# Optimization experiments

Measured on AMD Instinct MI355X. Metric: run time of the kernel, lower is better.

## Reference

```python
import jax, jax.numpy as jnp
import numpy as np

B, S, H_IN = 32, 1024, 1024
N_BLK, D_BLK = 64, 16
H_OUT = N_BLK * D_BLK  # 1024


def setup_inputs() -> dict:
    key = jax.random.key(0)
    ks = jax.random.split(key, 10)
    u = lambda k, shape: jax.random.uniform(k, shape, jnp.float32, -0.1, 0.1)
    return {
        "x": jax.random.normal(ks[0], (B, S, H_IN), jnp.float32),
        "h_0": jnp.zeros((B, H_OUT), jnp.float32),
        "c_0": jnp.zeros((B, N_BLK, D_BLK), jnp.float32),
        "Wi": u(ks[1], (N_BLK, H_IN)),
        "bi": jax.random.uniform(ks[2], (N_BLK,), jnp.float32, -1.0, 0.0),
        "Wo": u(ks[3], (N_BLK, H_IN)),
        "bo": jax.random.uniform(ks[4], (N_BLK,), jnp.float32, -1.0, 0.0),
        "Wg": u(ks[5], (H_OUT, H_IN)),
        "bg": u(ks[6], (H_OUT,)),
        "Ui": u(ks[7], (N_BLK, H_OUT)),
        "Uo": u(ks[8], (N_BLK, H_OUT)),
        "Ug": u(ks[9], (H_OUT, H_OUT)),
    }


def _lstm1997(x, h_0, c_0, Wi, bi, Wo, bo, Wg, bg, Ui, Uo, Ug):
    b, s, _ = x.shape
    n_blk, d_blk = c_0.shape[1], c_0.shape[2]
    # Precompute input-to-gate projections for all timesteps (same math, hoisted).
    xi = jnp.einsum("bsi,ni->bsn", x, Wi) + bi          # (B,S,nBlk)
    xo = jnp.einsum("bsi,ni->bsn", x, Wo) + bo          # (B,S,nBlk)
    xg = jnp.einsum("bsi,hi->bsh", x, Wg) + bg          # (B,S,hOut)

    def step(carry, inp):
        h, c = carry                                    # (B,hOut), (B,nBlk,dBlk)
        xi_t, xo_t, xg_t = inp
        i_t = jax.nn.sigmoid(xi_t + h @ Ui.T)           # (B,nBlk)
        o_t = jax.nn.sigmoid(xo_t + h @ Uo.T)           # (B,nBlk)
        g_t = jnp.tanh(xg_t + h @ Ug.T).reshape(b, n_blk, d_blk)
        c_new = c + i_t[:, :, None] * g_t               # (B,nBlk,dBlk)
        h_new = (o_t[:, :, None] * jnp.tanh(c_new)).reshape(b, n_blk * d_blk)
        return (h_new, c_new), (c_new, h_new)

    xs = (jnp.swapaxes(xi, 0, 1), jnp.swapaxes(xo, 0, 1), jnp.swapaxes(xg, 0, 1))
    _, (c_seq, h_seq) = jax.lax.scan(step, (h_0, c_0), xs)
    c = jnp.swapaxes(c_seq, 0, 1)                       # (B,S,nBlk,dBlk)
    h = jnp.swapaxes(h_seq, 0, 1)                       # (B,S,hOut)
    return c, h


def reference(x, h_0, c_0, Wi, bi, Wo, bo, Wg, bg, Ui, Uo, Ug):
    return _lstm1997(x, h_0, c_0, Wi, bi, Wo, bo, Wg, bg, Ui, Uo, Ug)
```

## Files before the change

kernel.cpp:

```cpp
#include <hip/hip_runtime.h>
#include <stdint.h>

#define B_    32
#define S_    1024
#define HIN   1024
#define NBLK  64
#define DBLK  16
#define HOUT  1024
#define NGATE 1152
#define NSLICE 32

typedef __attribute__((ext_vector_type(8))) __bf16 bf16x8;
typedef __attribute__((ext_vector_type(4))) float  f32x4;
typedef __attribute__((ext_vector_type(4))) unsigned int u32x4;

__device__ __forceinline__ unsigned short f2bf(float f) {
    union { float f; unsigned u; } v; v.f = f;
    return (unsigned short)((v.u + 0x7fffu + ((v.u >> 16) & 1u)) >> 16);
}
__device__ __forceinline__ float bf2f(unsigned short h) {
    union { unsigned u; float f; } v; v.u = ((unsigned)h) << 16; return v.f;
}
__device__ __forceinline__ void split1(float f, unsigned short& hi, unsigned short& lo) {
    hi = f2bf(f);
    lo = f2bf(f - bf2f(hi));
}

__device__ __forceinline__ int slice_row(int slice, int r) {
    return (r < 32) ? (128 + slice * 32 + r)
         : (r < 34) ? (slice * 2 + (r - 32))
                    : (64 + slice * 2 + (r - 34));
}


__global__ void k_init(const float* __restrict__ Wi, const float* __restrict__ Wo,
                       const float* __restrict__ Wg,
                       const float* __restrict__ Ui, const float* __restrict__ Uo,
                       const float* __restrict__ Ug, const float* __restrict__ h0,
                       unsigned short* __restrict__ WsH, unsigned short* __restrict__ WsL,
                       unsigned short* __restrict__ UsH, unsigned short* __restrict__ UsL,
                       unsigned short* __restrict__ hbH, unsigned short* __restrict__ hbL)
{
    int idx = blockIdx.x * 256 + threadIdx.x;
    const int nW = NGATE * HOUT / 4;
    float4 v; unsigned short *dH, *dL;
    if (idx < nW) {
        int f = idx * 4; int row = f >> 10, k = f & 1023;
        const float* src = (row < 64)  ? (Wi + (size_t)row * HIN)
                         : (row < 128) ? (Wo + (size_t)(row - 64) * HIN)
                                       : (Wg + (size_t)(row - 128) * HIN);
        v = *(const float4*)(src + k);
        dH = WsH + f; dL = WsL + f;
    } else if (idx < 2 * nW) {
        int f = (idx - nW) * 4; int row = f >> 10, k = f & 1023;
        const float* src = (row < 64)  ? (Ui + (size_t)row * HOUT)
                         : (row < 128) ? (Uo + (size_t)(row - 64) * HOUT)
                                       : (Ug + (size_t)(row - 128) * HOUT);
        v = *(const float4*)(src + k);
        dH = UsH + f; dL = UsL + f;
    } else {
        int f = (idx - 2 * nW) * 4;
        if (f >= B_ * HOUT) return;
        v = *(const float4*)(h0 + f);
        int b = f >> 10, c = f & 1023;
        int g = b >> 4, r = b & 15;
        int off = g * 16384 + (c >> 3) * 128 + r * 8 + (c & 7);
        unsigned short th[4], tl[4];
        split1(v.x, th[0], tl[0]); split1(v.y, th[1], tl[1]);
        split1(v.z, th[2], tl[2]); split1(v.w, th[3], tl[3]);
        __hip_atomic_store((unsigned*)(hbH + off), (unsigned)th[0] | ((unsigned)th[1] << 16),
                           __ATOMIC_RELAXED, __HIP_MEMORY_SCOPE_AGENT);
        __hip_atomic_store((unsigned*)(hbH + off) + 1, (unsigned)th[2] | ((unsigned)th[3] << 16),
                           __ATOMIC_RELAXED, __HIP_MEMORY_SCOPE_AGENT);
        __hip_atomic_store((unsigned*)(hbL + off), (unsigned)tl[0] | ((unsigned)tl[1] << 16),
                           __ATOMIC_RELAXED, __HIP_MEMORY_SCOPE_AGENT);
        __hip_atomic_store((unsigned*)(hbL + off) + 1, (unsigned)tl[2] | ((unsigned)tl[3] << 16),
                           __ATOMIC_RELAXED, __HIP_MEMORY_SCOPE_AGENT);
        return;
    }
    unsigned short th[4], tl[4];
    split1(v.x, th[0], tl[0]); split1(v.y, th[1], tl[1]);
    split1(v.z, th[2], tl[2]); split1(v.w, th[3], tl[3]);
    *(uint2*)dH = *(const uint2*)th;
    *(uint2*)dL = *(const uint2*)tl;
}

#define BM 128
#define BN 128
#define BK 32
#define LDP 56

__global__ __launch_bounds__(256) void k_gates(
    const float* __restrict__ x,
    const unsigned short* __restrict__ WsH, const unsigned short* __restrict__ WsL,
    const float* __restrict__ bi, const float* __restrict__ bo, const float* __restrict__ bg,
    float* __restrict__ c_out, float* __restrict__ h_out)
{
    __shared__ unsigned short AlH[BM][LDP], AlL[BM][LDP];
    __shared__ unsigned short BlH[BN][LDP], BlL[BN][LDP];
    const int tid  = threadIdx.x;
    const int bm   = blockIdx.x, bn = blockIdx.y;
    const int wave = tid >> 6,  lane = tid & 63;
    const int l15  = lane & 15, l4 = lane >> 4;
    const int wm   = wave >> 1, wn = wave & 1;
    const int rbase = tid >> 3;
    const int c4    = (tid & 7) * 4;

    f32x4 acc[4][4] = {};

    for (int kk = 0; kk < HIN; kk += BK) {
        #pragma unroll
        for (int i = 0; i < 4; ++i) {
            int row = rbase + 32 * i;
            float4 v = *(const float4*)(x + (size_t)(bm * BM + row) * HIN + kk + c4);
            unsigned short th[4], tl[4];
            split1(v.x, th[0], tl[0]); split1(v.y, th[1], tl[1]);
            split1(v.z, th[2], tl[2]); split1(v.w, th[3], tl[3]);
            *(uint2*)&AlH[row][c4] = *(const uint2*)th;
            *(uint2*)&AlL[row][c4] = *(const uint2*)tl;
            int n = bn * BN + row;
            *(uint2*)&BlH[row][c4] = *(const uint2*)(WsH + (size_t)n * HIN + kk + c4);
            *(uint2*)&BlL[row][c4] = *(const uint2*)(WsL + (size_t)n * HIN + kk + c4);
        }
        __syncthreads();
        uint4 ah[4], al[4], bh4[4], bl4[4];
        #pragma unroll
        for (int mi = 0; mi < 4; ++mi) {
            ah[mi] = *(const uint4*)&AlH[wm * 64 + mi * 16 + l15][l4 * 8];
            al[mi] = *(const uint4*)&AlL[wm * 64 + mi * 16 + l15][l4 * 8];
        }
        #pragma unroll
        for (int ni = 0; ni < 4; ++ni) {
            bh4[ni] = *(const uint4*)&BlH[wn * 64 + ni * 16 + l15][l4 * 8];
            bl4[ni] = *(const uint4*)&BlL[wn * 64 + ni * 16 + l15][l4 * 8];
        }
        #pragma unroll
        for (int mi = 0; mi < 4; ++mi) {
            #pragma unroll
            for (int ni = 0; ni < 4; ++ni) {
                acc[mi][ni] = __builtin_amdgcn_mfma_f32_16x16x32_bf16(
                    __builtin_bit_cast(bf16x8, ah[mi]), __builtin_bit_cast(bf16x8, bh4[ni]),
                    acc[mi][ni], 0, 0, 0);
                acc[mi][ni] = __builtin_amdgcn_mfma_f32_16x16x32_bf16(
                    __builtin_bit_cast(bf16x8, ah[mi]), __builtin_bit_cast(bf16x8, bl4[ni]),
                    acc[mi][ni], 0, 0, 0);
                acc[mi][ni] = __builtin_amdgcn_mfma_f32_16x16x32_bf16(
                    __builtin_bit_cast(bf16x8, al[mi]), __builtin_bit_cast(bf16x8, bh4[ni]),
                    acc[mi][ni], 0, 0, 0);
            }
        }
        __syncthreads();
    }

    #pragma unroll
    for (int ni = 0; ni < 4; ++ni) {
        int n = bn * BN + wn * 64 + ni * 16 + l15;
        float bv = (n < 64) ? bi[n] : (n < 128) ? bo[n - 64] : bg[n - 128];
        #pragma unroll
        for (int mi = 0; mi < 4; ++mi) {
            #pragma unroll
            for (int r = 0; r < 4; ++r) {
                int m = bm * BM + wm * 64 + mi * 16 + l4 * 4 + r;
                float val = acc[mi][ni][r] + bv;
                if (n >= 128) {
                    h_out[(size_t)m * HOUT + (n - 128)] = val;
                } else if (n < 64) {
                    c_out[((size_t)m * NBLK + n) * DBLK + 0] = val;
                } else {
                    c_out[((size_t)m * NBLK + (n - 64)) * DBLK + 1] = val;
                }
            }
        }
    }
}

__global__ __launch_bounds__(256, 1) void k_rec(
    const float* __restrict__ c0,
    float* __restrict__ c_out, float* __restrict__ h_out,
    const unsigned short* __restrict__ UsH, const unsigned short* __restrict__ UsL,
    unsigned short* __restrict__ hbH, unsigned short* __restrict__ hbL,
    unsigned int* __restrict__ flags)
{
    __shared__ unsigned short Wlo[37][1032];
    __shared__ float preW[4][16][53];

    const int tid   = threadIdx.x;
    const int slice = blockIdx.x & 31;
    const int group = blockIdx.x >> 5;
    const int wave  = tid >> 6, lane = tid & 63;
    const int l15   = lane & 15, l4 = lane >> 4;

    for (int idx = tid; idx < 37 * 128; idx += 256) {
        int row = idx >> 7, c8 = idx & 127;
        uint4 v = make_uint4(0, 0, 0, 0);
        if (row < 36)
            v = *(const uint4*)(UsL + (size_t)slice_row(slice, row) * HOUT + c8 * 8);
        *(uint4*)&Wlo[row][c8 * 8] = v;
    }

    int wrow[3];
    uint4 bwh[3][8];
    #pragma unroll
    for (int nt = 0; nt < 3; ++nt) {
        int grow = nt * 16 + l15;
        bool valid = grow < 36;
        wrow[nt] = valid ? grow : 36;
        int srow = valid ? slice_row(slice, grow) : 0;
        const unsigned short* ph = UsH + (size_t)srow * HOUT + wave * 256 + l4 * 8;
        #pragma unroll
        for (int ks = 0; ks < 8; ++ks)
            bwh[nt][ks] = valid ? *(const uint4*)(ph + ks * 32) : make_uint4(0, 0, 0, 0);
    }

    const int e0   = tid * 2;
    const int bl   = e0 >> 5;
    const int col0 = e0 & 31;
    const int Bg   = group * 16 + bl;
    const int hcol = slice * 32 + col0;
    const int blkI = hcol >> 4, d0 = hcol & 15;
    float cr0 = c0[((size_t)Bg * NBLK + blkI) * DBLK + d0];
    float cr1 = c0[((size_t)Bg * NBLK + blkI) * DBLK + d0 + 1];

    const int puboff = group * 16384 + (slice * 4 + (col0 >> 3)) * 128 + bl * 8 + (col0 & 7);

    unsigned int* flagbase = flags + (size_t)group * NSLICE * 32;
    unsigned int* myflag   = flagbase + slice * 32;
    unsigned int* pollfl   = flagbase + (lane & 31) * 32;

    const int abase = ((wave * 32 + l4) * 128 + l15 * 8);

    float xg0, xg1, xi, xo;
    {
        size_t r0 = (size_t)Bg * S_;
        xg0 = h_out[r0 * HOUT + hcol];
        xg1 = h_out[r0 * HOUT + hcol + 1];
        xi  = c_out[(r0 * NBLK + blkI) * DBLK + 0];
        xo  = c_out[(r0 * NBLK + blkI) * DBLK + 1];
    }

    __syncthreads();

    for (int t = 0; t < S_; ++t) {
        if (t > 0) {
            if (wave == 0) {
                unsigned v;
                do {
                    v = __hip_atomic_load(pollfl, __ATOMIC_RELAXED, __HIP_MEMORY_SCOPE_AGENT);
                } while (!__all((int)(v >= (unsigned)t)));
            }
            __syncthreads();
        }

        u32x4 ah[8], al[8];
        {
            const char* pH = (const char*)(hbH + (size_t)(t & 1) * 32768
                                           + group * 16384 + abase);
            const char* pL = (const char*)(hbL + (size_t)(t & 1) * 32768
                                           + group * 16384 + abase);
            asm volatile(
                "global_load_dwordx4 %0, %16, off sc0 sc1\n\t"
                "global_load_dwordx4 %1, %16, off offset:1024 sc0 sc1\n\t"
                "global_load_dwordx4 %2, %16, off offset:2048 sc0 sc1\n\t"
                "global_load_dwordx4 %3, %16, off offset:3072 sc0 sc1\n\t"
                "global_load_dwordx4 %4, %17, off sc0 sc1\n\t"
                "global_load_dwordx4 %5, %17, off offset:1024 sc0 sc1\n\t"
                "global_load_dwordx4 %6, %17, off offset:2048 sc0 sc1\n\t"
                "global_load_dwordx4 %7, %17, off offset:3072 sc0 sc1\n\t"
                "global_load_dwordx4 %8, %18, off sc0 sc1\n\t"
                "global_load_dwordx4 %9, %18, off offset:1024 sc0 sc1\n\t"
                "global_load_dwordx4 %10, %18, off offset:2048 sc0 sc1\n\t"
                "global_load_dwordx4 %11, %18, off offset:3072 sc0 sc1\n\t"
                "global_load_dwordx4 %12, %19, off sc0 sc1\n\t"
                "global_load_dwordx4 %13, %19, off offset:1024 sc0 sc1\n\t"
                "global_load_dwordx4 %14, %19, off offset:2048 sc0 sc1\n\t"
                "global_load_dwordx4 %15, %19, off offset:3072 sc0 sc1\n\t"
                "s_waitcnt vmcnt(0)\n\t"
                : "=&v"(ah[0]), "=&v"(ah[1]), "=&v"(ah[2]), "=&v"(ah[3]),
                  "=&v"(ah[4]), "=&v"(ah[5]), "=&v"(ah[6]), "=&v"(ah[7]),
                  "=&v"(al[0]), "=&v"(al[1]), "=&v"(al[2]), "=&v"(al[3]),
                  "=&v"(al[4]), "=&v"(al[5]), "=&v"(al[6]), "=&v"(al[7])
                : "v"(pH), "v"(pH + 4096), "v"(pL), "v"(pL + 4096)
                : "memory");
            __builtin_amdgcn_sched_barrier(0);
        }

        float nxg0 = 0.f, nxg1 = 0.f, nxi = 0.f, nxo = 0.f;
        if (t + 1 < S_) {
            size_t rn = (size_t)Bg * S_ + (t + 1);
            nxg0 = h_out[rn * HOUT + hcol];
            nxg1 = h_out[rn * HOUT + hcol + 1];
            nxi  = c_out[(rn * NBLK + blkI) * DBLK + 0];
            nxo  = c_out[(rn * NBLK + blkI) * DBLK + 1];
        }

        f32x4 acc[3] = {};
        #pragma unroll
        for (int ks = 0; ks < 8; ++ks) {
            #pragma unroll
            for (int nt = 0; nt < 3; ++nt) {
                uint4 bl_ = *(const uint4*)&Wlo[wrow[nt]][wave * 256 + ks * 32 + l4 * 8];
                acc[nt] = __builtin_amdgcn_mfma_f32_16x16x32_bf16(
                        __builtin_bit_cast(bf16x8, ah[ks]), __builtin_bit_cast(bf16x8, bwh[nt][ks]), acc[nt], 0, 0, 0);
                acc[nt] = __builtin_amdgcn_mfma_f32_16x16x32_bf16(
                        __builtin_bit_cast(bf16x8, al[ks]), __builtin_bit_cast(bf16x8, bwh[nt][ks]), acc[nt], 0, 0, 0);
                acc[nt] = __builtin_amdgcn_mfma_f32_16x16x32_bf16(
                        __builtin_bit_cast(bf16x8, ah[ks]), __builtin_bit_cast(bf16x8, bl_), acc[nt], 0, 0, 0);
            }
        }

        #pragma unroll
        for (int nt = 0; nt < 3; ++nt) {
            #pragma unroll
            for (int r = 0; r < 4; ++r)
                preW[wave][l4 * 4 + r][nt * 16 + l15] = acc[nt][r];
        }
        __syncthreads();

        float gp0 = xg0, gp1 = xg1, ip = xi, op = xo;
        #pragma unroll
        for (int w = 0; w < 4; ++w) {
            gp0 += preW[w][bl][col0];
            gp1 += preW[w][bl][col0 + 1];
            ip  += preW[w][bl][32 + (col0 >> 4)];
            op  += preW[w][bl][34 + (col0 >> 4)];
        }
        float ig  = 1.f / (1.f + __expf(-ip));
        float og  = 1.f / (1.f + __expf(-op));
        cr0 += ig * tanhf(gp0);
        cr1 += ig * tanhf(gp1);
        float h0v = og * tanhf(cr0);
        float h1v = og * tanhf(cr1);

        unsigned short h0h, h0l, h1h, h1l;
        split1(h0v, h0h, h0l); split1(h1v, h1h, h1l);
        size_t dsto = (size_t)((t + 1) & 1) * 32768 + puboff;
        __hip_atomic_store((unsigned int*)(hbH + dsto),
                           (unsigned)h0h | ((unsigned)h1h << 16),
                           __ATOMIC_RELAXED, __HIP_MEMORY_SCOPE_AGENT);
        __hip_atomic_store((unsigned int*)(hbL + dsto),
                           (unsigned)h0l | ((unsigned)h1l << 16),
                           __ATOMIC_RELAXED, __HIP_MEMORY_SCOPE_AGENT);

        asm volatile("s_waitcnt vmcnt(0)" ::: "memory");
        __syncthreads();
        if (tid == 64)
            __hip_atomic_store(myflag, (unsigned)(t + 1),
                               __ATOMIC_RELAXED, __HIP_MEMORY_SCOPE_AGENT);

        size_t ro = (size_t)Bg * S_ + t;
        c_out[(ro * NBLK + blkI) * DBLK + d0]     = cr0;
        c_out[(ro * NBLK + blkI) * DBLK + d0 + 1] = cr1;
        h_out[ro * HOUT + hcol]     = h0v;
        h_out[ro * HOUT + hcol + 1] = h1v;

        xg0 = nxg0; xg1 = nxg1; xi = nxi; xo = nxo;
    }
}

extern "C" void kernel_launch(void* const* d_in, const int* in_sizes, int n_in,
                              void* d_out, int out_size, void* d_ws, size_t ws_size,
                              hipStream_t stream) {
    const float* x  = (const float*)d_in[0];
    const float* h0 = (const float*)d_in[1];
    const float* c0 = (const float*)d_in[2];
    const float* Wi = (const float*)d_in[3];
    const float* bi = (const float*)d_in[4];
    const float* Wo = (const float*)d_in[5];
    const float* bo = (const float*)d_in[6];
    const float* Wg = (const float*)d_in[7];
    const float* bg = (const float*)d_in[8];
    const float* Ui = (const float*)d_in[9];
    const float* Uo = (const float*)d_in[10];
    const float* Ug = (const float*)d_in[11];

    float* c_out = (float*)d_out;
    float* h_out = c_out + (size_t)B_ * S_ * NBLK * DBLK;

    unsigned short* WsH  = (unsigned short*)d_ws;
    unsigned short* WsL  = WsH + (size_t)NGATE * HOUT;
    unsigned short* UsH  = WsL + (size_t)NGATE * HOUT;
    unsigned short* UsL  = UsH + (size_t)NGATE * HOUT;
    unsigned short* hbH  = UsL + (size_t)NGATE * HOUT;
    unsigned short* hbL  = hbH + (size_t)2 * B_ * HOUT;
    unsigned int*   flags = (unsigned int*)(hbL + (size_t)2 * B_ * HOUT);

    hipMemsetAsync(flags, 0, 64 * 32 * sizeof(unsigned int), stream);
    k_init<<<2336, 256, 0, stream>>>(Wi, Wo, Wg, Ui, Uo, Ug, h0, WsH, WsL, UsH, UsL, hbH, hbL);
    k_gates<<<dim3((B_ * S_) / BM, NGATE / BN), 256, 0, stream>>>(
        x, WsH, WsL, bi, bo, bg, c_out, h_out);
    k_rec<<<64, 256, 0, stream>>>(c0, c_out, h_out, UsH, UsL, hbH, hbL, flags);
}
```

Measured before the change: 3.788 ms.

## Fold both batch groups into each recurrent block, halving the persistent grid

Before the change the recurrent kernel ran 64 blocks, one per (slice, batch group) pair. Now it runs 32 blocks, and each block processes both 16-row batch groups one after the other inside each timestep. The same register- and LDS-resident weights serve both groups, so the weight footprint per CU halves and fewer blocks take part in the grid-wide flag handshake. In exchange each block does twice the serial work per step, and the two groups' wait–compute–publish phases are interleaved rather than overlapped on separate CUs. This may lengthen the per-step critical path.

```diff
diff --git a/kernel.cpp b/kernel.cpp
--- a/kernel.cpp
+++ b/kernel.cpp
@@ -185,8 +185,7 @@
     __shared__ float preW[4][16][53];
 
     const int tid   = threadIdx.x;
-    const int slice = blockIdx.x & 31;
-    const int group = blockIdx.x >> 5;
+    const int slice = blockIdx.x;
     const int wave  = tid >> 6, lane = tid & 63;
     const int l15   = lane & 15, l4 = lane >> 4;
 
@@ -215,145 +214,148 @@
     const int e0   = tid * 2;
     const int bl   = e0 >> 5;
     const int col0 = e0 & 31;
-    const int Bg   = group * 16 + bl;
     const int hcol = slice * 32 + col0;
     const int blkI = hcol >> 4, d0 = hcol & 15;
-    float cr0 = c0[((size_t)Bg * NBLK + blkI) * DBLK + d0];
-    float cr1 = c0[((size_t)Bg * NBLK + blkI) * DBLK + d0 + 1];
-
-    const int puboff = group * 16384 + (slice * 4 + (col0 >> 3)) * 128 + bl * 8 + (col0 & 7);
-
-    unsigned int* flagbase = flags + (size_t)group * NSLICE * 32;
-    unsigned int* myflag   = flagbase + slice * 32;
-    unsigned int* pollfl   = flagbase + (lane & 31) * 32;
+
+    float cr0[2], cr1[2], xg0[2], xg1[2], xiv[2], xov[2];
+    #pragma unroll
+    for (int g = 0; g < 2; ++g) {
+        int Bg = g * 16 + bl;
+        cr0[g] = c0[((size_t)Bg * NBLK + blkI) * DBLK + d0];
+        cr1[g] = c0[((size_t)Bg * NBLK + blkI) * DBLK + d0 + 1];
+        size_t r0 = (size_t)Bg * S_;
+        xg0[g] = h_out[r0 * HOUT + hcol];
+        xg1[g] = h_out[r0 * HOUT + hcol + 1];
+        xiv[g] = c_out[(r0 * NBLK + blkI) * DBLK + 0];
+        xov[g] = c_out[(r0 * NBLK + blkI) * DBLK + 1];
+    }
 
     const int abase = ((wave * 32 + l4) * 128 + l15 * 8);
 
-    float xg0, xg1, xi, xo;
-    {
-        size_t r0 = (size_t)Bg * S_;
-        xg0 = h_out[r0 * HOUT + hcol];
-        xg1 = h_out[r0 * HOUT + hcol + 1];
-        xi  = c_out[(r0 * NBLK + blkI) * DBLK + 0];
-        xo  = c_out[(r0 * NBLK + blkI) * DBLK + 1];
-    }
-
     __syncthreads();
 
     for (int t = 0; t < S_; ++t) {
-        if (t > 0) {
-            if (wave == 0) {
-                unsigned v;
-                do {
-                    v = __hip_atomic_load(pollfl, __ATOMIC_RELAXED, __HIP_MEMORY_SCOPE_AGENT);
-                } while (!__all((int)(v >= (unsigned)t)));
+        #pragma unroll
+        for (int g = 0; g < 2; ++g) {
+            unsigned int* flagbase = flags + (size_t)g * NSLICE * 32;
+            const int Bg = g * 16 + bl;
+
+            if (t > 0) {
+                if (wave == 0) {
+                    unsigned int* pollfl = flagbase + (lane & 31) * 32;
+                    unsigned v;
+                    do {
+                        v = __hip_atomic_load(pollfl, __ATOMIC_RELAXED, __HIP_MEMORY_SCOPE_AGENT);
+                    } while (!__all((int)(v >= (unsigned)t)));
+                }
+                __syncthreads();
+            }
+
+            u32x4 ah[8], al[8];
+            {
+                const char* pH = (const char*)(hbH + (size_t)(t & 1) * 32768
+                                               + g * 16384 + abase);
+                const char* pL = (const char*)(hbL + (size_t)(t & 1) * 32768
+                                               + g * 16384 + abase);
+                asm volatile(
+                    "global_load_dwordx4 %0, %16, off sc0 sc1\n\t"
+                    "global_load_dwordx4 %1, %16, off offset:1024 sc0 sc1\n\t"
+                    "global_load_dwordx4 %2, %16, off offset:2048 sc0 sc1\n\t"
+                    "global_load_dwordx4 %3, %16, off offset:3072 sc0 sc1\n\t"
+                    "global_load_dwordx4 %4, %17, off sc0 sc1\n\t"
+                    "global_load_dwordx4 %5, %17, off offset:1024 sc0 sc1\n\t"
+                    "global_load_dwordx4 %6, %17, off offset:2048 sc0 sc1\n\t"
+                    "global_load_dwordx4 %7, %17, off offset:3072 sc0 sc1\n\t"
+                    "global_load_dwordx4 %8, %18, off sc0 sc1\n\t"
+                    "global_load_dwordx4 %9, %18, off offset:1024 sc0 sc1\n\t"
+                    "global_load_dwordx4 %10, %18, off offset:2048 sc0 sc1\n\t"
+                    "global_load_dwordx4 %11, %18, off offset:3072 sc0 sc1\n\t"
+                    "global_load_dwordx4 %12, %19, off sc0 sc1\n\t"
+                    "global_load_dwordx4 %13, %19, off offset:1024 sc0 sc1\n\t"
+                    "global_load_dwordx4 %14, %19, off offset:2048 sc0 sc1\n\t"
+                    "global_load_dwordx4 %15, %19, off offset:3072 sc0 sc1\n\t"
+                    "s_waitcnt vmcnt(0)\n\t"
+                    : "=&v"(ah[0]), "=&v"(ah[1]), "=&v"(ah[2]), "=&v"(ah[3]),
+                      "=&v"(ah[4]), "=&v"(ah[5]), "=&v"(ah[6]), "=&v"(ah[7]),
+                      "=&v"(al[0]), "=&v"(al[1]), "=&v"(al[2]), "=&v"(al[3]),
+                      "=&v"(al[4]), "=&v"(al[5]), "=&v"(al[6]), "=&v"(al[7])
+                    : "v"(pH), "v"(pH + 4096), "v"(pL), "v"(pL + 4096)
+                    : "memory");
+                __builtin_amdgcn_sched_barrier(0);
+            }
+
+            float nxg0 = 0.f, nxg1 = 0.f, nxi = 0.f, nxo = 0.f;
+            if (t + 1 < S_) {
+                size_t rn = (size_t)Bg * S_ + (t + 1);
+                nxg0 = h_out[rn * HOUT + hcol];
+                nxg1 = h_out[rn * HOUT + hcol + 1];
+                nxi  = c_out[(rn * NBLK + blkI) * DBLK + 0];
+                nxo  = c_out[(rn * NBLK + blkI) * DBLK + 1];
+            }
+
+            f32x4 acc[3] = {};
+            #pragma unroll
+            for (int ks = 0; ks < 8; ++ks) {
+                #pragma unroll
+                for (int nt = 0; nt < 3; ++nt) {
+                    uint4 bl_ = *(const uint4*)&Wlo[wrow[nt]][wave * 256 + ks * 32 + l4 * 8];
+                    acc[nt] = __builtin_amdgcn_mfma_f32_16x16x32_bf16(
+                            __builtin_bit_cast(bf16x8, ah[ks]), __builtin_bit_cast(bf16x8, bwh[nt][ks]), acc[nt], 0, 0, 0);
+                    acc[nt] = __builtin_amdgcn_mfma_f32_16x16x32_bf16(
+                            __builtin_bit_cast(bf16x8, al[ks]), __builtin_bit_cast(bf16x8, bwh[nt][ks]), acc[nt], 0, 0, 0);
+                    acc[nt] = __builtin_amdgcn_mfma_f32_16x16x32_bf16(
+                            __builtin_bit_cast(bf16x8, ah[ks]), __builtin_bit_cast(bf16x8, bl_), acc[nt], 0, 0, 0);
+                }
+            }
+
+            #pragma unroll
+            for (int nt = 0; nt < 3; ++nt) {
+                #pragma unroll
+                for (int r = 0; r < 4; ++r)
+                    preW[wave][l4 * 4 + r][nt * 16 + l15] = acc[nt][r];
             }
             __syncthreads();
-        }
-
-        u32x4 ah[8], al[8];
-        {
-            const char* pH = (const char*)(hbH + (size_t)(t & 1) * 32768
-                                           + group * 16384 + abase);
-            const char* pL = (const char*)(hbL + (size_t)(t & 1) * 32768
-                                           + group * 16384 + abase);
-            asm volatile(
-                "global_load_dwordx4 %0, %16, off sc0 sc1\n\t"
-                "global_load_dwordx4 %1, %16, off offset:1024 sc0 sc1\n\t"
-                "global_load_dwordx4 %2, %16, off offset:2048 sc0 sc1\n\t"
-                "global_load_dwordx4 %3, %16, off offset:3072 sc0 sc1\n\t"
-                "global_load_dwordx4 %4, %17, off sc0 sc1\n\t"
-                "global_load_dwordx4 %5, %17, off offset:1024 sc0 sc1\n\t"
-                "global_load_dwordx4 %6, %17, off offset:2048 sc0 sc1\n\t"
-                "global_load_dwordx4 %7, %17, off offset:3072 sc0 sc1\n\t"
-                "global_load_dwordx4 %8, %18, off sc0 sc1\n\t"
-                "global_load_dwordx4 %9, %18, off offset:1024 sc0 sc1\n\t"
-                "global_load_dwordx4 %10, %18, off offset:2048 sc0 sc1\n\t"
-                "global_load_dwordx4 %11, %18, off offset:3072 sc0 sc1\n\t"
-                "global_load_dwordx4 %12, %19, off sc0 sc1\n\t"
-                "global_load_dwordx4 %13, %19, off offset:1024 sc0 sc1\n\t"
-                "global_load_dwordx4 %14, %19, off offset:2048 sc0 sc1\n\t"
-                "global_load_dwordx4 %15, %19, off offset:3072 sc0 sc1\n\t"
-                "s_waitcnt vmcnt(0)\n\t"
-                : "=&v"(ah[0]), "=&v"(ah[1]), "=&v"(ah[2]), "=&v"(ah[3]),
-                  "=&v"(ah[4]), "=&v"(ah[5]), "=&v"(ah[6]), "=&v"(ah[7]),
-                  "=&v"(al[0]), "=&v"(al[1]), "=&v"(al[2]), "=&v"(al[3]),
-                  "=&v"(al[4]), "=&v"(al[5]), "=&v"(al[6]), "=&v"(al[7])
-                : "v"(pH), "v"(pH + 4096), "v"(pL), "v"(pL + 4096)
-                : "memory");
-            __builtin_amdgcn_sched_barrier(0);
-        }
-
-        float nxg0 = 0.f, nxg1 = 0.f, nxi = 0.f, nxo = 0.f;
-        if (t + 1 < S_) {
-            size_t rn = (size_t)Bg * S_ + (t + 1);
-            nxg0 = h_out[rn * HOUT + hcol];
-            nxg1 = h_out[rn * HOUT + hcol + 1];
-            nxi  = c_out[(rn * NBLK + blkI) * DBLK + 0];
-            nxo  = c_out[(rn * NBLK + blkI) * DBLK + 1];
-        }
-
-        f32x4 acc[3] = {};
-        #pragma unroll
-        for (int ks = 0; ks < 8; ++ks) {
-            #pragma unroll
-            for (int nt = 0; nt < 3; ++nt) {
-                uint4 bl_ = *(const uint4*)&Wlo[wrow[nt]][wave * 256 + ks * 32 + l4 * 8];
-                acc[nt] = __builtin_amdgcn_mfma_f32_16x16x32_bf16(
-                        __builtin_bit_cast(bf16x8, ah[ks]), __builtin_bit_cast(bf16x8, bwh[nt][ks]), acc[nt], 0, 0, 0);
-                acc[nt] = __builtin_amdgcn_mfma_f32_16x16x32_bf16(
-                        __builtin_bit_cast(bf16x8, al[ks]), __builtin_bit_cast(bf16x8, bwh[nt][ks]), acc[nt], 0, 0, 0);
-                acc[nt] = __builtin_amdgcn_mfma_f32_16x16x32_bf16(
-                        __builtin_bit_cast(bf16x8, ah[ks]), __builtin_bit_cast(bf16x8, bl_), acc[nt], 0, 0, 0);
-            }
-        }
-
-        #pragma unroll
-        for (int nt = 0; nt < 3; ++nt) {
-            #pragma unroll
-            for (int r = 0; r < 4; ++r)
-                preW[wave][l4 * 4 + r][nt * 16 + l15] = acc[nt][r];
-        }
-        __syncthreads();
-
-        float gp0 = xg0, gp1 = xg1, ip = xi, op = xo;
-        #pragma unroll
-        for (int w = 0; w < 4; ++w) {
-            gp0 += preW[w][bl][col0];
-            gp1 += preW[w][bl][col0 + 1];
-            ip  += preW[w][bl][32 + (col0 >> 4)];
-            op  += preW[w][bl][34 + (col0 >> 4)];
-        }
-        float ig  = 1.f / (1.f + __expf(-ip));
-        float og  = 1.f / (1.f + __expf(-op));
-        cr0 += ig * tanhf(gp0);
-        cr1 += ig * tanhf(gp1);
-        float h0v = og * tanhf(cr0);
-        float h1v = og * tanhf(cr1);
-
-        unsigned short h0h, h0l, h1h, h1l;
-        split1(h0v, h0h, h0l); split1(h1v, h1h, h1l);
-        size_t dsto = (size_t)((t + 1) & 1) * 32768 + puboff;
-        __hip_atomic_store((unsigned int*)(hbH + dsto),
-                           (unsigned)h0h | ((unsigned)h1h << 16),
-                           __ATOMIC_RELAXED, __HIP_MEMORY_SCOPE_AGENT);
-        __hip_atomic_store((unsigned int*)(hbL + dsto),
-                           (unsigned)h0l | ((unsigned)h1l << 16),
-                           __ATOMIC_RELAXED, __HIP_MEMORY_SCOPE_AGENT);
-
-        asm volatile("s_waitcnt vmcnt(0)" ::: "memory");
-        __syncthreads();
-        if (tid == 64)
-            __hip_atomic_store(myflag, (unsigned)(t + 1),
+
+            float gp0 = xg0[g], gp1 = xg1[g], ip = xiv[g], op = xov[g];
+            #pragma unroll
+            for (int w = 0; w < 4; ++w) {
+                gp0 += preW[w][bl][col0];
+                gp1 += preW[w][bl][col0 + 1];
+                ip  += preW[w][bl][32 + (col0 >> 4)];
+                op  += preW[w][bl][34 + (col0 >> 4)];
+            }
+            float ig  = 1.f / (1.f + __expf(-ip));
+            float og  = 1.f / (1.f + __expf(-op));
+            cr0[g] += ig * tanhf(gp0);
+            cr1[g] += ig * tanhf(gp1);
+            float h0v = og * tanhf(cr0[g]);
+            float h1v = og * tanhf(cr1[g]);
+
+            unsigned short h0h, h0l, h1h, h1l;
+            split1(h0v, h0h, h0l); split1(h1v, h1h, h1l);
+            size_t dsto = (size_t)((t + 1) & 1) * 32768 + g * 16384
+                        + (slice * 4 + (col0 >> 3)) * 128 + bl * 8 + (col0 & 7);
+            __hip_atomic_store((unsigned int*)(hbH + dsto),
+                               (unsigned)h0h | ((unsigned)h1h << 16),
                                __ATOMIC_RELAXED, __HIP_MEMORY_SCOPE_AGENT);
-
-        size_t ro = (size_t)Bg * S_ + t;
-        c_out[(ro * NBLK + blkI) * DBLK + d0]     = cr0;
-        c_out[(ro * NBLK + blkI) * DBLK + d0 + 1] = cr1;
-        h_out[ro * HOUT + hcol]     = h0v;
-        h_out[ro * HOUT + hcol + 1] = h1v;
-
-        xg0 = nxg0; xg1 = nxg1; xi = nxi; xo = nxo;
+            __hip_atomic_store((unsigned int*)(hbL + dsto),
+                               (unsigned)h0l | ((unsigned)h1l << 16),
+                               __ATOMIC_RELAXED, __HIP_MEMORY_SCOPE_AGENT);
+
+            asm volatile("s_waitcnt vmcnt(0)" ::: "memory");
+            __syncthreads();
+            if (tid == 64)
+                __hip_atomic_store(flagbase + slice * 32, (unsigned)(t + 1),
+                                   __ATOMIC_RELAXED, __HIP_MEMORY_SCOPE_AGENT);
+
+            size_t ro = (size_t)Bg * S_ + t;
+            c_out[(ro * NBLK + blkI) * DBLK + d0]     = cr0[g];
+            c_out[(ro * NBLK + blkI) * DBLK + d0 + 1] = cr1[g];
+            h_out[ro * HOUT + hcol]     = h0v;
+            h_out[ro * HOUT + hcol + 1] = h1v;
+
+            xg0[g] = nxg0; xg1[g] = nxg1; xiv[g] = nxi; xov[g] = nxo;
+        }
     }
 }
 
@@ -388,5 +390,5 @@
     k_init<<<2336, 256, 0, stream>>>(Wi, Wo, Wg, Ui, Uo, Ug, h0, WsH, WsL, UsH, UsL, hbH, hbL);
     k_gates<<<dim3((B_ * S_) / BM, NGATE / BN), 256, 0, stream>>>(
         x, WsH, WsL, bi, bo, bg, c_out, h_out);
-    k_rec<<<64, 256, 0, stream>>>(c0, c_out, h_out, UsH, UsL, hbH, hbL, flags);
-}
+    k_rec<<<32, 256, 0, stream>>>(c0, c_out, h_out, UsH, UsL, hbH, hbL, flags);
+}
```

New measurement: 6.233 ms. 64.6% more time.
